# Kernel tuning notes

Hardware: AMD Instinct MI355X
Metric: run time of the kernel (lower is better)

## Reference

```python
import jax, jax.numpy as jnp
import numpy as np

B, S, D = 32, 2048, 768   # batch, seq_len, hidden_dim
NL, NF = 512, 64          # num_lines, num_functions


def setup_inputs() -> dict:
    key = jax.random.key(0)
    k = jax.random.split(key, 4)
    hidden_states = jax.random.normal(k[0], (B, S, D), dtype=jnp.float32)
    proj_W = jax.random.normal(k[1], (D, D), dtype=jnp.float32) * 0.02
    proj_b = jnp.zeros((D,), dtype=jnp.float32)
    # start <= end per pair, indices in-range
    line_boundaries = jnp.sort(jax.random.randint(k[2], (B, NL, 2), 0, S), axis=-1)
    function_boundaries = jnp.sort(jax.random.randint(k[3], (B, NF, 2), 0, NL), axis=-1)
    return dict(hidden_states=hidden_states, proj_W=proj_W, proj_b=proj_b,
                line_boundaries=line_boundaries, function_boundaries=function_boundaries)


def segment_mean(x, boundaries):
    """Mean of x[b, start:end] per segment; zeros when start >= end.
    x: [B, S, D]; boundaries: [B, N, 2] -> [B, N, D].
    Uses an exclusive prefix-sum so all segments are reduced in one pass."""
    csum = jnp.concatenate([jnp.zeros_like(x[:, :1]), jnp.cumsum(x, axis=1)], axis=1)  # [B, S+1, D]
    start = boundaries[..., 0]
    end = boundaries[..., 1]
    take = lambda idx: jnp.take_along_axis(csum, idx[..., None], axis=1)  # [B, N, D]
    seg_sum = take(end) - take(start)
    length = (end - start).astype(x.dtype)[..., None]
    return jnp.where(length > 0, seg_sum / jnp.maximum(length, 1.0), jnp.zeros_like(seg_sum))


def reference(hidden_states, proj_W, proj_b, line_boundaries, function_boundaries):
    # CodeEncoder projection of pretrained hidden states (no complexity features)
    token_emb = hidden_states @ proj_W + proj_b                     # [B, S, D]
    # _encode_lines: per-boundary token mean
    line_emb = segment_mean(token_emb, line_boundaries)             # [B, NL, D]
    # _encode_functions: per-boundary line mean
    func_emb = segment_mean(line_emb, function_boundaries)          # [B, NF, D]
    # AdaptiveAvgPool1d(1) over the function axis
    file_emb = jnp.mean(func_emb, axis=1)                           # [B, D]
    return token_emb, line_emb, func_emb, file_emb
```

## Files before the change

kernel.cpp:

```cpp
#include <hip/hip_runtime.h>

#define Bq 32
#define Sq 2048
#define Dq 768
#define NLq 512
#define NFq 64
#define SCHUNKS 16
#define LCHUNKS 8

typedef unsigned short u16;
typedef unsigned int u32;
typedef __attribute__((ext_vector_type(4))) unsigned short us4;
typedef __attribute__((ext_vector_type(4))) unsigned int u32x4;
typedef __attribute__((ext_vector_type(8))) short s16x8;
typedef __attribute__((ext_vector_type(4))) float f32x4;

static __device__ __forceinline__ u16 f2bf(float f) {
  unsigned int u = __builtin_bit_cast(unsigned int, f);
  u += 0x7fffu + ((u >> 16) & 1u);
  return (u16)(u >> 16);
}

static __device__ __forceinline__ void gload16(const void* g, void* l) {
  __builtin_amdgcn_global_load_lds(
      (const __attribute__((address_space(1))) unsigned int*)g,
      (__attribute__((address_space(3))) unsigned int*)l, 16, 0, 0);
}

__global__ __launch_bounds__(256) void wt_kernel(const float* __restrict__ W,
                                                 u16* __restrict__ Wt) {
  int idx = blockIdx.x * 256 + threadIdx.x;
  int n = idx / Dq, k = idx % Dq;
  Wt[idx] = f2bf(W[(size_t)k * Dq + n]);
}

__global__ __launch_bounds__(256, 3) void gemm_kernel(const float* __restrict__ A,
                                                      const u16* __restrict__ Wt,
                                                      const float* __restrict__ bias,
                                                      float* __restrict__ C,
                                                      float* __restrict__ pre,
                                                      float* __restrict__ part16) {
  __shared__ float Asf[128 * 32];
  __shared__ u16 Bs[128 * 32];
  __shared__ float ps[2][128];
  const int tid = threadIdx.x;
  const int gn0 = blockIdx.x * 128;
  const int gm0 = blockIdx.y * 128;
  const int wave = tid >> 6, lane = tid & 63;
  const int lm = lane & 15, quad = lane >> 4;
  const int wm = (wave & 1) * 64, wn = (wave >> 1) * 64;

  const int arow = tid >> 3;
  const int ah = (tid & 7) ^ (arow & 7);
  const size_t astride = (size_t)Dq * 4;
  const char* ga = (const char*)A + (size_t)(gm0 + arow) * astride + ah * 16;
  const char* gb0 = (const char*)Wt + (size_t)(gn0 + (tid >> 2)) * (Dq * 2) + (tid & 3) * 16;
  const char* gb1 = gb0 + (size_t)64 * (Dq * 2);
  char* lA = (char*)Asf + wave * 1024;
  char* lB = (char*)Bs + wave * 1024;

  f32x4 acc[4][4] = {};
  const int ax = lm & 7;

  for (int kk = 0; kk < Dq / 32; ++kk) {
    __syncthreads();
    gload16(ga, lA);
    gload16(ga + 32 * astride, lA + 4096);
    gload16(ga + 64 * astride, lA + 8192);
    gload16(ga + 96 * astride, lA + 12288);
    gload16(gb0, lB);
    gload16(gb1, lB + 4096);
    ga += 128; gb0 += 64; gb1 += 64;
    __syncthreads();

    s16x8 af[4], bfr[4];
#pragma unroll
    for (int i = 0; i < 4; ++i) {
      const float* rowA = Asf + (wm + i * 16 + lm) * 32;
      f32x4 alo = *(const f32x4*)(rowA + (((2 * quad) ^ ax) << 2));
      f32x4 ahi = *(const f32x4*)(rowA + (((2 * quad + 1) ^ ax) << 2));
      u32 p0, p1, p2, p3;
      asm("v_cvt_pk_bf16_f32 %0, %1, %2" : "=v"(p0) : "v"(alo.x), "v"(alo.y));
      asm("v_cvt_pk_bf16_f32 %0, %1, %2" : "=v"(p1) : "v"(alo.z), "v"(alo.w));
      asm("v_cvt_pk_bf16_f32 %0, %1, %2" : "=v"(p2) : "v"(ahi.x), "v"(ahi.y));
      asm("v_cvt_pk_bf16_f32 %0, %1, %2" : "=v"(p3) : "v"(ahi.z), "v"(ahi.w));
      u32x4 u;
      u.x = p0; u.y = p1; u.z = p2; u.w = p3;
      af[i] = __builtin_bit_cast(s16x8, u);
    }
#pragma unroll
    for (int i = 0; i < 4; ++i)
      bfr[i] = *(const s16x8*)&Bs[(wn + i * 16 + lm) * 32 + quad * 8];
#pragma unroll
    for (int mi = 0; mi < 4; ++mi)
#pragma unroll
      for (int ni = 0; ni < 4; ++ni)
        acc[mi][ni] = __builtin_amdgcn_mfma_f32_16x16x32_bf16(af[mi], bfr[ni],
                                                              acc[mi][ni], 0, 0, 0);
  }

#pragma unroll
  for (int ni = 0; ni < 4; ++ni) {
    const int gn = gn0 + wn + ni * 16 + lm;
    const float bv = bias[gn];
    float psum = 0.f;
#pragma unroll
    for (int mi = 0; mi < 4; ++mi) {
#pragma unroll
      for (int r = 0; r < 4; ++r) {
        const int gm = gm0 + wm + mi * 16 + quad * 4 + r;
        const float cv = acc[mi][ni][r] + bv;
        C[(size_t)gm * Dq + gn] = cv;
        psum += cv;
      }
    }
    psum += __shfl_xor(psum, 16);
    psum += __shfl_xor(psum, 32);
    if (lane < 16) ps[wave & 1][wn + ni * 16 + lm] = psum;
  }
  __syncthreads();
  if (tid < 128) {
    const int b = gm0 >> 11;
    const int sc = (gm0 >> 7) & 15;
    part16[((size_t)b * SCHUNKS + sc) * Dq + gn0 + tid] = ps[0][tid] + ps[1][tid];
  }

#pragma unroll
  for (int ni = 0; ni < 4; ++ni) {
    const int col = wn + ni * 16 + lm;
    const float bv = bias[gn0 + col];
    float em = wm ? ps[0][col] : 0.f;
#pragma unroll
    for (int mi = 0; mi < 4; ++mi) {
      const float v0 = acc[mi][ni][0] + bv, v1 = acc[mi][ni][1] + bv,
                  v2 = acc[mi][ni][2] + bv, v3 = acc[mi][ni][3] + bv;
      const float qs = v0 + v1 + v2 + v3;
      const float t1 = __shfl_up(qs, 16);
      const float i1 = qs + (quad >= 1 ? t1 : 0.f);
      const float t2 = __shfl_up(i1, 32);
      const float iq = i1 + (quad >= 2 ? t2 : 0.f);
      const float eq = iq - qs;
      const float tot = __shfl(iq, 48 + lm);
      const float base = em + eq;
      em += tot;
      const float P0 = base + v0, P1 = P0 + v1, P2 = P1 + v2, P3 = P2 + v3;
      const size_t rowb = (size_t)(gm0 + wm + mi * 16 + quad * 4) * Dq + gn0 + col;
      pre[rowb] = P0;
      pre[rowb + Dq] = P1;
      pre[rowb + 2 * (size_t)Dq] = P2;
      pre[rowb + 3 * (size_t)Dq] = P3;
    }
  }
}

__global__ __launch_bounds__(256) void scan_kernel(float* __restrict__ p, int C) {
  const int idx = blockIdx.x * 256 + threadIdx.x;
  const int b = idx / Dq, d = idx % Dq;
  float run = 0.f;
  for (int c = 0; c < C; ++c) {
    const size_t o = ((size_t)b * C + c) * Dq + d;
    const float v = p[o];
    p[o] = run;
    run += v;
  }
}

__global__ __launch_bounds__(64) void line_kernel(const float* __restrict__ pre,
                                                  const float* __restrict__ part,
                                                  const int* __restrict__ lb,
                                                  float* __restrict__ lemb,
                                                  float* __restrict__ lpart) {
  __shared__ int sb[128];
  __shared__ float soff[SCHUNKS][64];
  const int lc = blockIdx.x, d64 = blockIdx.y, b = blockIdx.z;
  const int tid = threadIdx.x;
  if (tid < 32)
    ((int4*)sb)[tid] = ((const int4*)(lb + ((size_t)b * NLq + lc * 64) * 2))[tid];
  const int d = d64 * 64 + tid;
#pragma unroll
  for (int sc = 0; sc < SCHUNKS; ++sc)
    soff[sc][tid] = part[((size_t)b * SCHUNKS + sc) * Dq + d];
  __syncthreads();
  const float* pb = pre + (size_t)b * Sq * Dq + d;
  float* le = lemb + ((size_t)b * NLq + lc * 64) * Dq + d;
  float sum = 0.f;
  for (int n0 = 0; n0 < 64; n0 += 8) {
    float vs[8], ve[8];
    int len[8];
#pragma unroll
    for (int i = 0; i < 8; ++i) {
      const int s0 = sb[2 * (n0 + i)], s1 = sb[2 * (n0 + i) + 1];
      len[i] = s1 - s0;
      const int t0 = s0 > 0 ? s0 - 1 : 0;
      const int t1 = s1 > 0 ? s1 - 1 : 0;
      const float a0 = pb[(size_t)t0 * Dq] + soff[t0 >> 7][tid];
      const float a1 = pb[(size_t)t1 * Dq] + soff[t1 >> 7][tid];
      vs[i] = s0 > 0 ? a0 : 0.f;
      ve[i] = a1;
    }
#pragma unroll
    for (int i = 0; i < 8; ++i) {
      const float v = len[i] > 0 ? (ve[i] - vs[i]) / (float)len[i] : 0.f;
      le[(size_t)(n0 + i) * Dq] = v;
      sum += v;
    }
  }
  lpart[((size_t)b * LCHUNKS + lc) * Dq + d] = sum;
}

__global__ __launch_bounds__(256) void lcsum_kernel(const float* __restrict__ lemb,
                                                    const float* __restrict__ lpart,
                                                    float* __restrict__ lcsum) {
  const int lc = blockIdx.x, dc = blockIdx.y, b = blockIdx.z;
  const int d = dc * 256 + threadIdx.x;
  const float* src = lemb + ((size_t)b * NLq + lc * 64) * Dq + d;
  float* dst = lcsum + ((size_t)b * (NLq + 1) + lc * 64 + 1) * Dq + d;
  float run = lpart[((size_t)b * LCHUNKS + lc) * Dq + d];
  if (lc == 0) lcsum[(size_t)b * (NLq + 1) * Dq + d] = 0.f;
  for (int n0 = 0; n0 < 64; n0 += 8) {
    float v[8];
#pragma unroll
    for (int i = 0; i < 8; ++i) v[i] = src[(size_t)(n0 + i) * Dq];
#pragma unroll
    for (int i = 0; i < 8; ++i) {
      run += v[i];
      dst[(size_t)(n0 + i) * Dq] = run;
    }
  }
}

__global__ __launch_bounds__(64) void func_kernel(const float* __restrict__ lcsum,
                                                  const int* __restrict__ fb,
                                                  float* __restrict__ femb,
                                                  float* __restrict__ file) {
  __shared__ int sb[NFq * 2];
  const int tid = threadIdx.x;
  const int d64 = blockIdx.x, b = blockIdx.y;
  const int d = d64 * 64 + tid;
  if (tid < NFq * 2 / 4)
    ((int4*)sb)[tid] = ((const int4*)(fb + (size_t)b * NFq * 2))[tid];
  __syncthreads();
  const float* lc = lcsum + (size_t)b * (NLq + 1) * Dq + d;
  float* fe = femb + (size_t)b * NFq * Dq + d;
  float acc = 0.f;
#pragma unroll 8
  for (int f = 0; f < NFq; ++f) {
    const int l0 = sb[2 * f], l1 = sb[2 * f + 1];
    const float v = l1 > l0 ? (lc[(size_t)l1 * Dq] - lc[(size_t)l0 * Dq]) / (float)(l1 - l0)
                            : 0.f;
    fe[(size_t)f * Dq] = v;
    acc += v;
  }
  file[(size_t)b * Dq + d] = acc * (1.f / (float)NFq);
}

extern "C" void kernel_launch(void* const* d_in, const int* in_sizes, int n_in,
                              void* d_out, int out_size, void* d_ws, size_t ws_size,
                              hipStream_t stream) {
  const float* hs   = (const float*)d_in[0];
  const float* W    = (const float*)d_in[1];
  const float* bias = (const float*)d_in[2];
  const int* lb     = (const int*)d_in[3];
  const int* fb     = (const int*)d_in[4];

  float* out = (float*)d_out;
  float* token = out;
  float* line  = token + (size_t)Bq * Sq * Dq;
  float* func  = line + (size_t)Bq * NLq * Dq;
  float* file  = func + (size_t)Bq * NFq * Dq;

  char* ws = (char*)d_ws;
  float* precsum = (float*)ws;
  float* lcsum   = (float*)(ws + 201498624);
  float* part16  = lcsum;
  u16*   Wt      = (u16*)(ws + 201498624 + 50442240);
  float* lpart   = (float*)Wt;

  wt_kernel<<<(Dq * Dq) / 256, 256, 0, stream>>>(W, Wt);
  gemm_kernel<<<dim3(Dq / 128, (Bq * Sq) / 128), 256, 0, stream>>>(hs, Wt, bias, token,
                                                                   precsum, part16);
  scan_kernel<<<(Bq * Dq) / 256, 256, 0, stream>>>(part16, SCHUNKS);
  line_kernel<<<dim3(LCHUNKS, 12, Bq), 64, 0, stream>>>(precsum, part16, lb, line, lpart);
  scan_kernel<<<(Bq * Dq) / 256, 256, 0, stream>>>(lpart, LCHUNKS);
  lcsum_kernel<<<dim3(LCHUNKS, 3, Bq), 256, 0, stream>>>(line, lpart, lcsum);
  func_kernel<<<dim3(12, Bq), 64, 0, stream>>>(lcsum, fb, func, file);
}
```

Before: 690.6 us.

## Double-buffer GEMM LDS tiles and remap block IDs across XCDs

The GEMM main loop now uses two LDS buffers for the A and B tiles. The next K-slice is prefetched with global_load_lds while MFMAs run on the current slice, which removes one barrier per iteration and overlaps loading with compute. Block indices are also remapped so that neighbouring output tiles, which share rows of A, go to the same XCD, to improve L2 reuse. Doubling the LDS tiles raises shared-memory use per block, which may limit how many blocks fit on each CU.

```diff
diff --git a/kernel.cpp b/kernel.cpp
--- a/kernel.cpp
+++ b/kernel.cpp
@@ -40,12 +40,14 @@
                                                       float* __restrict__ C,
                                                       float* __restrict__ pre,
                                                       float* __restrict__ part16) {
-  __shared__ float Asf[128 * 32];
-  __shared__ u16 Bs[128 * 32];
+  __shared__ float Asf[2][128 * 32];
+  __shared__ u16 Bs[2][128 * 32];
   __shared__ float ps[2][128];
   const int tid = threadIdx.x;
-  const int gn0 = blockIdx.x * 128;
-  const int gm0 = blockIdx.y * 128;
+  const int bid = blockIdx.y * gridDim.x + blockIdx.x;
+  const int lid = (bid & 7) * 384 + (bid >> 3);
+  const int gn0 = (lid % 6) * 128;
+  const int gm0 = (lid / 6) * 128;
   const int wave = tid >> 6, lane = tid & 63;
   const int lm = lane & 15, quad = lane >> 4;
   const int wm = (wave & 1) * 64, wn = (wave >> 1) * 64;
@@ -56,27 +58,33 @@
   const char* ga = (const char*)A + (size_t)(gm0 + arow) * astride + ah * 16;
   const char* gb0 = (const char*)Wt + (size_t)(gn0 + (tid >> 2)) * (Dq * 2) + (tid & 3) * 16;
   const char* gb1 = gb0 + (size_t)64 * (Dq * 2);
-  char* lA = (char*)Asf + wave * 1024;
-  char* lB = (char*)Bs + wave * 1024;
 
   f32x4 acc[4][4] = {};
   const int ax = lm & 7;
 
-  for (int kk = 0; kk < Dq / 32; ++kk) {
-    __syncthreads();
-    gload16(ga, lA);
-    gload16(ga + 32 * astride, lA + 4096);
-    gload16(ga + 64 * astride, lA + 8192);
-    gload16(ga + 96 * astride, lA + 12288);
-    gload16(gb0, lB);
-    gload16(gb1, lB + 4096);
-    ga += 128; gb0 += 64; gb1 += 64;
-    __syncthreads();
+  auto stage = [&](int t, int buf) {
+    char* lA = (char*)&Asf[buf][0] + wave * 1024;
+    char* lB = (char*)&Bs[buf][0] + wave * 1024;
+    const char* gat = ga + t * 128;
+    gload16(gat, lA);
+    gload16(gat + 32 * astride, lA + 4096);
+    gload16(gat + 64 * astride, lA + 8192);
+    gload16(gat + 96 * astride, lA + 12288);
+    gload16(gb0 + t * 64, lB);
+    gload16(gb1 + t * 64, lB + 4096);
+  };
+
+  stage(0, 0);
+  __syncthreads();
+
+  for (int t = 0; t < Dq / 32; ++t) {
+    if (t < Dq / 32 - 1) stage(t + 1, (t + 1) & 1);
+    const int buf = t & 1;
 
     s16x8 af[4], bfr[4];
 #pragma unroll
     for (int i = 0; i < 4; ++i) {
-      const float* rowA = Asf + (wm + i * 16 + lm) * 32;
+      const float* rowA = &Asf[buf][(wm + i * 16 + lm) * 32];
       f32x4 alo = *(const f32x4*)(rowA + (((2 * quad) ^ ax) << 2));
       f32x4 ahi = *(const f32x4*)(rowA + (((2 * quad + 1) ^ ax) << 2));
       u32 p0, p1, p2, p3;
@@ -90,13 +98,14 @@
     }
 #pragma unroll
     for (int i = 0; i < 4; ++i)
-      bfr[i] = *(const s16x8*)&Bs[(wn + i * 16 + lm) * 32 + quad * 8];
+      bfr[i] = *(const s16x8*)&Bs[buf][(wn + i * 16 + lm) * 32 + quad * 8];
 #pragma unroll
     for (int mi = 0; mi < 4; ++mi)
 #pragma unroll
       for (int ni = 0; ni < 4; ++ni)
         acc[mi][ni] = __builtin_amdgcn_mfma_f32_16x16x32_bf16(af[mi], bfr[ni],
                                                               acc[mi][ni], 0, 0, 0);
+    __syncthreads();
   }
 
 #pragma unroll
```

After: 650.0 us. -5.9%, faster.
